# Kernel tuning notes

Hardware: AMD Instinct MI355X
Metric: run time of the kernel (lower is better)

The kernel has to match this reference:

```python
import jax, jax.numpy as jnp
import numpy as np

B, N, E = 2, 50000, 800000
IN_CH, SP_CH, OUT_CH, EDGE_CH = 64, 16, 32, 1


def _xavier(k, shape):
    scale = (2.0 / (shape[0] + shape[1])) ** 0.5
    return jax.random.normal(k, shape, dtype=jnp.float32) * scale


def setup_inputs() -> dict:
    key = jax.random.key(0)
    ks = jax.random.split(key, 20)
    return {
        "X": jax.random.normal(ks[0], (B, N, IN_CH), dtype=jnp.float32),
        "edge_index0": jax.random.randint(ks[1], (2, E), 0, N),
        "edge_index1": jax.random.randint(ks[2], (2, E), 0, N),
        "edge_weight0": jax.random.uniform(ks[3], (E, EDGE_CH), dtype=jnp.float32),
        "edge_weight1": jax.random.uniform(ks[4], (E, EDGE_CH), dtype=jnp.float32),
        "res_n_id0": jnp.arange(N),
        "res_n_id1": jnp.arange(N),
        # conv1 params (in=IN_CH, out=SP_CH)
        "value1": _xavier(ks[5], (IN_CH, SP_CH)),
        "key1": _xavier(ks[6], (SP_CH, SP_CH)),
        "query1": _xavier(ks[7], (SP_CH, SP_CH)),
        "we1": _xavier(ks[8], (EDGE_CH, SP_CH)),
        "att_w1": _xavier(ks[9], (3 * SP_CH, 1)),
        "att_b1": jnp.zeros((1,), jnp.float32),
        "cat_w1": _xavier(ks[10], (2 * SP_CH, SP_CH)),
        "cat_b1": jnp.zeros((SP_CH,), jnp.float32),
        # conv2 params (in=SP_CH, out=OUT_CH)
        "value2": _xavier(ks[11], (SP_CH, OUT_CH)),
        "key2": _xavier(ks[12], (OUT_CH, OUT_CH)),
        "query2": _xavier(ks[13], (OUT_CH, OUT_CH)),
        "we2": _xavier(ks[14], (EDGE_CH, OUT_CH)),
        "att_w2": _xavier(ks[15], (3 * OUT_CH, 1)),
        "att_b2": jnp.zeros((1,), jnp.float32),
        "cat_w2": _xavier(ks[16], (2 * OUT_CH, OUT_CH)),
        "cat_b2": jnp.zeros((OUT_CH,), jnp.float32),
    }


def _egnn_conv(Xs, Xd, ei, ef, value, key_w, query_w, we, att_w, att_b, cat_w, cat_b):
    # Xs: [B,Ns,Cin] source nodes, Xd: [B,Nd,Cin] dest nodes, ei: [2,E], ef: [E,edge_ch]
    xs = Xs @ value                       # [B,Ns,C]
    xd = Xd @ value                       # [B,Nd,C]
    e = ef @ we                           # [E,C]
    xj = xs[:, ei[0]]                     # [B,E,C] source gather
    xi = xd[:, ei[1]]                     # [B,E,C] dest gather
    q = xj @ query_w                      # note: original code names are swapped; kept faithful
    k = xi @ key_w
    att_in = jnp.concatenate([k, q, jnp.broadcast_to(e, q.shape)], axis=-1)  # [B,E,3C]
    att = jax.nn.sigmoid(att_in @ att_w + att_b)      # [B,E,1]
    msg = att * xj * jax.nn.sigmoid(e)                # [B,E,C]
    aggr = jnp.zeros(xd.shape, xd.dtype).at[:, ei[1]].add(msg)  # scatter-add over dest
    upd = jnp.concatenate([xd, aggr], axis=-1) @ cat_w + cat_b  # [B,Nd,C]
    return xd + jax.nn.relu(upd)


def reference(X, edge_index0, edge_index1, edge_weight0, edge_weight1,
              res_n_id0, res_n_id1,
              value1, key1, query1, we1, att_w1, att_b1, cat_w1, cat_b1,
              value2, key2, query2, we2, att_w2, att_b2, cat_w2, cat_b2):
    X1 = _egnn_conv(X, X[:, res_n_id0], edge_index0, edge_weight0,
                    value1, key1, query1, we1, att_w1, att_b1, cat_w1, cat_b1)
    X1 = jax.nn.leaky_relu(X1)  # negative_slope 0.01, matches torch default
    X2 = _egnn_conv(X1, X1[:, res_n_id1], edge_index1, edge_weight1,
                    value2, key2, query2, we2, att_w2, att_b2, cat_w2, cat_b2)
    return X2
```

## Files before the change

kernel.cpp:

```cpp
#include <hip/hip_runtime.h>
#include <hip/hip_fp16.h>

#define BB   2
#define NN   50000
#define EE   800000
#define INCH 64
#define C1   16
#define C2   32
#define NB   (BB*NN)

#define W1S   6
#define W2S   5
#define NBK1  ((NN + 63) >> 6)
#define NBK2  ((NN + 31) >> 5)
#define NBKT  (NBK1 + NBK2)
#define EB    4096
#define TPB   1024
#define NEBLK ((2*EE + EB - 1) / EB)

#define OFF_XS1   0
#define OFF_XS2   (OFF_XS1 + NB*C1/2)
#define OFF_DOTK1 (OFF_XS2 + NB*C2/2)
#define OFF_DOTQ1 (OFF_DOTK1 + NB)
#define OFF_DOTK2 (OFF_DOTQ1 + NB)
#define OFF_DOTQ2 (OFF_DOTK2 + NB)
#define OFF_AG1   (OFF_DOTQ2 + NB)
#define OFF_AG2   (OFF_AG1 + NN*32)
#define OFF_BTOT  (OFF_AG2 + NN*64)
#define OFF_BBASE (OFF_BTOT + NBKT)
#define OFF_START (OFF_BBASE + NBKT)
#define OFF_DEG   (OFF_START + 2*NN)
#define OFF_SC    (OFF_DEG + 2*NN)
#define OFF_RECS2 (OFF_SC + 2)
#define OFF_REGION (OFF_RECS2 + 2*EE*2)
#define OFF_RECS   OFF_REGION
#define OFF_BCNT   (OFF_REGION + 2*EE*2)
#define OFF_PREC   OFF_REGION

__device__ __forceinline__ float sigmoidf(float x) {
    return __builtin_amdgcn_rcpf(1.0f + __expf(-x));
}

__global__ void k_sc(const float* __restrict__ we1, const float* __restrict__ aw1,
                     const float* __restrict__ we2, const float* __restrict__ aw2,
                     float* __restrict__ sc) {
    if (threadIdx.x == 0) {
        float e = 0.f;
        for (int j = 0; j < C1; ++j) e += we1[j] * aw1[2*C1+j];
        sc[0] = e;
    }
    if (threadIdx.x == 1) {
        float e = 0.f;
        for (int j = 0; j < C2; ++j) e += we2[j] * aw2[2*C2+j];
        sc[1] = e;
    }
}

__global__ __launch_bounds__(TPB) void k_cnt(
        const int* __restrict__ ei0, const int* __restrict__ ei1,
        unsigned* __restrict__ blockCnt) {
    __shared__ unsigned h[NBKT];
    int tid = threadIdx.x;
    for (int i = tid; i < NBKT; i += TPB) h[i] = 0u;
    __syncthreads();
    int base = blockIdx.x * EB;
#pragma unroll
    for (int j = 0; j < EB/TPB; ++j) {
        int t = base + j*TPB + tid;
        if (t < 2*EE) {
            int bkt;
            if (t < EE) { int dst = ei0[EE + t];      bkt = dst >> W1S; }
            else        { int dst = ei1[EE + t - EE]; bkt = NBK1 + (dst >> W2S); }
            atomicAdd(&h[bkt], 1u);
        }
    }
    __syncthreads();
    unsigned* o = blockCnt + (size_t)blockIdx.x * NBKT;
    for (int i = tid; i < NBKT; i += TPB) o[i] = h[i];
}

__global__ __launch_bounds__(512) void k_scanBkt(
        unsigned* __restrict__ blockCnt, unsigned* __restrict__ bktTot) {
    __shared__ unsigned s[512];
    int tid = threadIdx.x;
    int bkt = blockIdx.x;
    unsigned v = (tid < NEBLK) ? blockCnt[(size_t)tid * NBKT + bkt] : 0u;
    s[tid] = v;
    __syncthreads();
    for (int o = 1; o < 512; o <<= 1) {
        unsigned t = (tid >= o) ? s[tid - o] : 0u;
        __syncthreads();
        s[tid] += t;
        __syncthreads();
    }
    if (tid < NEBLK) blockCnt[(size_t)tid * NBKT + bkt] = s[tid] - v;
    if (tid == 511) bktTot[bkt] = s[511];
}

__global__ __launch_bounds__(1024) void k_scanTot(
        const unsigned* __restrict__ bktTot, unsigned* __restrict__ bucketBase) {
    __shared__ unsigned s[1024];
    int tid = threadIdx.x;
    int base = tid * 3;
    unsigned a0 = (base + 0 < NBKT) ? bktTot[base + 0] : 0u;
    unsigned a1 = (base + 1 < NBKT) ? bktTot[base + 1] : 0u;
    unsigned a2 = (base + 2 < NBKT) ? bktTot[base + 2] : 0u;
    unsigned l = a0 + a1 + a2;
    s[tid] = l;
    __syncthreads();
    for (int o = 1; o < 1024; o <<= 1) {
        unsigned t = (tid >= o) ? s[tid - o] : 0u;
        __syncthreads();
        s[tid] += t;
        __syncthreads();
    }
    unsigned ex = s[tid] - l;
    if (base + 0 < NBKT) bucketBase[base + 0] = ex;
    if (base + 1 < NBKT) bucketBase[base + 1] = ex + a0;
    if (base + 2 < NBKT) bucketBase[base + 2] = ex + a0 + a1;
}

__global__ __launch_bounds__(TPB) void k_permute(
        const int* __restrict__ ei0, const int* __restrict__ ei1,
        const float* __restrict__ ew0, const float* __restrict__ ew1,
        const unsigned* __restrict__ blockOff, const unsigned* __restrict__ bucketBase,
        uint2* __restrict__ recs) {
    __shared__ unsigned off[NBKT];
    __shared__ unsigned cur[NBKT];
    int tid = threadIdx.x;
    const unsigned* bo = blockOff + (size_t)blockIdx.x * NBKT;
    for (int i = tid; i < NBKT; i += TPB) { off[i] = bo[i] + bucketBase[i]; cur[i] = 0u; }
    __syncthreads();
    int base = blockIdx.x * EB;
#pragma unroll
    for (int j = 0; j < EB/TPB; ++j) {
        int t = base + j*TPB + tid;
        if (t >= 2*EE) break;
        int bkt, dl, src; float ef;
        if (t < EE) {
            int dst = ei0[EE + t];
            bkt = dst >> W1S; dl = dst & 63;
            src = ei0[t]; ef = ew0[t];
        } else {
            int e = t - EE;
            int dst = ei1[EE + e];
            bkt = NBK1 + (dst >> W2S); dl = dst & 31;
            src = ei1[e]; ef = ew1[e];
        }
        unsigned pos = off[bkt] + atomicAdd(&cur[bkt], 1u);
        recs[pos] = make_uint2((unsigned)src | ((unsigned)dl << 16), __float_as_uint(ef));
    }
}

__global__ __launch_bounds__(256) void k_sortb(
        const uint2* __restrict__ recs, const unsigned* __restrict__ bktTot,
        const unsigned* __restrict__ bucketBase,
        uint2* __restrict__ recs2, unsigned* __restrict__ startA,
        unsigned* __restrict__ degA) {
    __shared__ unsigned h[64], sOff[64], cur[64];
    int tid = threadIdx.x;
    int bkt = blockIdx.x;
    int lay1 = (bkt < NBK1) ? 1 : 0;
    int ndl  = lay1 ? 64 : 32;
    int nodeBase = lay1 ? (bkt << W1S) : ((bkt - NBK1) << W2S);
    int layOff   = lay1 ? 0 : NN;
    if (tid < 64) h[tid] = 0u;
    __syncthreads();
    unsigned cnt = bktTot[bkt], base = bucketBase[bkt];
    for (unsigned i = tid; i < cnt; i += 256)
        atomicAdd(&h[recs[base + i].x >> 16], 1u);
    __syncthreads();
    if (tid == 0) {
        unsigned run = 0;
        for (int d = 0; d < ndl; ++d) { sOff[d] = run; run += h[d]; }
    }
    __syncthreads();
    if (tid < ndl) {
        cur[tid] = sOff[tid];
        int node = nodeBase + tid;
        if (node < NN) {
            startA[layOff + node] = base + sOff[tid];
            degA[layOff + node]   = h[tid];
        }
    }
    __syncthreads();
    for (unsigned i = tid; i < cnt; i += 256) {
        uint2 r = recs[base + i];
        unsigned dl  = r.x >> 16;
        unsigned src = r.x & 0xffffu;
        unsigned pos = atomicAdd(&cur[dl], 1u);
        unsigned dst = (unsigned)nodeBase + dl;
        recs2[base + pos] = make_uint2(src | (dst << 16), r.y);
    }
}

__global__ __launch_bounds__(256) void k_value1(
        const float* __restrict__ X, const float* __restrict__ value1,
        const float* __restrict__ key1, const float* __restrict__ query1,
        const float* __restrict__ aw1,
        __half* __restrict__ xs1h, float* __restrict__ dotk1, float* __restrict__ dotq1) {
    __shared__ float W[INCH*C1];
    __shared__ float KV[C1], QV[C1];
    int tid = threadIdx.x;
    for (int i = tid; i < INCH*C1; i += 256) W[i] = value1[i];
    if (tid < C1) {
        float kv = 0.f, qv = 0.f;
#pragma unroll
        for (int j = 0; j < C1; ++j) {
            kv += key1[tid*C1+j]   * aw1[j];
            qv += query1[tid*C1+j] * aw1[C1+j];
        }
        KV[tid] = kv; QV[tid] = qv;
    }
    __syncthreads();
    int bn = blockIdx.x * 256 + tid;
    if (bn >= NB) return;
    int b = (bn >= NN) ? 1 : 0;
    int node = bn - b*NN;
    const float4* Xr = (const float4*)(X + (size_t)bn * INCH);
    float acc[C1];
#pragma unroll
    for (int j = 0; j < C1; ++j) acc[j] = 0.f;
#pragma unroll
    for (int v = 0; v < 16; ++v) {
        float4 p = Xr[v];
        float x4[4] = {p.x, p.y, p.z, p.w};
#pragma unroll
        for (int h = 0; h < 4; ++h) {
            int i = v*4 + h;
            float xv = x4[h];
#pragma unroll
            for (int j = 0; j < C1; ++j) acc[j] += xv * W[i*C1+j];
        }
    }
    float dk = 0.f, dq = 0.f;
#pragma unroll
    for (int j = 0; j < C1; ++j) { dk += acc[j]*KV[j]; dq += acc[j]*QV[j]; }
    __half* o = xs1h + ((size_t)node * C1) * 2 + b;
#pragma unroll
    for (int j = 0; j < C1; ++j) o[2*j] = __float2half_rn(acc[j]);
    dotk1[node*2 + b] = dk; dotq1[node*2 + b] = dq;
}

__global__ __launch_bounds__(256) void k_prep(
        const uint2* __restrict__ recs2seg, const float* __restrict__ dotk,
        const float* __restrict__ dotq, const float* __restrict__ ab,
        const float* __restrict__ sc, int scIdx, uint2* __restrict__ prec) {
    int e = blockIdx.x * 256 + threadIdx.x;
    uint2 r = recs2seg[e];
    int src = r.x & 0xffff, dst = r.x >> 16;
    float ef = __uint_as_float(r.y);
    float eb = ef * sc[scIdx] + ab[0];
    float2 dk = *(const float2*)(dotk + dst*2);
    float2 dq = *(const float2*)(dotq + src*2);
    float p0 = sigmoidf(dk.x + dq.x + eb);
    float p1 = sigmoidf(dk.y + dq.y + eb);
    unsigned pu = __builtin_bit_cast(unsigned, __floats2half2_rn(p0, p1));
    unsigned eu = (unsigned)__half_as_ushort(__float2half_rn(ef));
    prec[e] = make_uint2((unsigned)src | (pu << 16),
                         (pu >> 16) | (eu << 16));
}

__global__ __launch_bounds__(256) void k_aggr1f(
        const uint2* __restrict__ prec, const float* __restrict__ we,
        const uint2* __restrict__ xsh,
        const unsigned* __restrict__ startA, const unsigned* __restrict__ degA,
        float* __restrict__ aggrf) {
    int t = blockIdx.x * 256 + threadIdx.x;
    int node = t >> 3, cp = t & 7;
    if (node >= NN) return;
    unsigned s = startA[node];
    unsigned n = degA[node];
    float w0 = we[2*cp], w1 = we[2*cp+1];
    float a0 = 0.f, a1 = 0.f, a2 = 0.f, a3 = 0.f;
    uint2 r_n = make_uint2(0u, 0u); uint2 xr_n = make_uint2(0u, 0u);
    if (n > 0) {
        r_n = prec[s];
        xr_n = xsh[(size_t)(r_n.x & 0xffff)*8 + cp];
    }
    for (unsigned i = 0; i < n; ++i) {
        uint2 r = r_n; uint2 xr = xr_n;
        if (i + 1 < n) {
            r_n = prec[s + i + 1];
            xr_n = xsh[(size_t)(r_n.x & 0xffff)*8 + cp];
        }
        float p0 = __half2float(__ushort_as_half((unsigned short)(r.x >> 16)));
        float p1 = __half2float(__ushort_as_half((unsigned short)(r.y & 0xffff)));
        float ef = __half2float(__ushort_as_half((unsigned short)(r.y >> 16)));
        float se0 = sigmoidf(ef * w0);
        float se1 = sigmoidf(ef * w1);
        float2 f0 = __half22float2(__builtin_bit_cast(__half2, xr.x));
        float2 f1 = __half22float2(__builtin_bit_cast(__half2, xr.y));
        a0 += p0 * se0 * f0.x;
        a1 += p1 * se0 * f0.y;
        a2 += p0 * se1 * f1.x;
        a3 += p1 * se1 * f1.y;
    }
    ((float4*)aggrf)[(size_t)node*8 + cp] = make_float4(a0, a1, a2, a3);
}

__global__ __launch_bounds__(256) void k_update1(
        const float* __restrict__ cat_w, const float* __restrict__ cat_b,
        const float* __restrict__ value2,
        const float* __restrict__ key2, const float* __restrict__ query2,
        const float* __restrict__ aw2,
        const __half* __restrict__ xs1h, const float* __restrict__ aggr1f,
        __half* __restrict__ xs2h, float* __restrict__ dotk2, float* __restrict__ dotq2) {
    __shared__ float CW[2*C1*C1];
    __shared__ float CB[C1];
    __shared__ float V2[C1*C2];
    __shared__ float KV[C2], QV[C2];
    int tid = threadIdx.x;
    for (int i = tid; i < 2*C1*C1; i += 256) CW[i] = cat_w[i];
    for (int i = tid; i < C1*C2;   i += 256) V2[i] = value2[i];
    if (tid < C1) CB[tid] = cat_b[tid];
    if (tid < C2) {
        float kv = 0.f;
#pragma unroll
        for (int j = 0; j < C2; ++j) kv += key2[tid*C2+j] * aw2[j];
        KV[tid] = kv;
    } else if (tid < 2*C2) {
        int c = tid - C2;
        float qv = 0.f;
#pragma unroll
        for (int j = 0; j < C2; ++j) qv += query2[c*C2+j] * aw2[C2+j];
        QV[c] = qv;
    }
    __syncthreads();
    int bn = blockIdx.x * 256 + tid;
    if (bn >= NB) return;
    int b = (bn >= NN) ? 1 : 0;
    int node = bn - b*NN;
    const __half* xr = xs1h + ((size_t)node*C1)*2 + b;
    const float* agp = aggr1f + (size_t)node*32;
    float xd[C1], ag[C1];
#pragma unroll
    for (int i = 0; i < C1; ++i) xd[i] = __half2float(xr[2*i]);
#pragma unroll
    for (int i = 0; i < C1; ++i) ag[i] = agp[(i>>1)*4 + (i&1)*2 + b];
    float x1[C1];
#pragma unroll
    for (int j = 0; j < C1; ++j) {
        float u = CB[j];
#pragma unroll
        for (int i = 0; i < C1; ++i) {
            u += xd[i] * CW[i*C1 + j];
            u += ag[i] * CW[(C1+i)*C1 + j];
        }
        float o = xd[j] + fmaxf(u, 0.f);
        x1[j] = (o > 0.f) ? o : 0.01f * o;
    }
    float o2[C2];
#pragma unroll
    for (int k = 0; k < C2; ++k) o2[k] = 0.f;
#pragma unroll
    for (int j = 0; j < C1; ++j) {
        float xv = x1[j];
#pragma unroll
        for (int k = 0; k < C2; ++k) o2[k] += xv * V2[j*C2 + k];
    }
    float dk = 0.f, dq = 0.f;
#pragma unroll
    for (int k = 0; k < C2; ++k) { dk += o2[k]*KV[k]; dq += o2[k]*QV[k]; }
    __half* o = xs2h + ((size_t)node*C2)*2 + b;
#pragma unroll
    for (int k = 0; k < C2; ++k) o[2*k] = __float2half_rn(o2[k]);
    dotk2[node*2 + b] = dk; dotq2[node*2 + b] = dq;
}

__global__ __launch_bounds__(256) void k_aggr2f(
        const uint2* __restrict__ prec, const float* __restrict__ we,
        const uint2* __restrict__ xsh,
        const unsigned* __restrict__ startA, const unsigned* __restrict__ degA,
        float* __restrict__ aggrf) {
    int t = blockIdx.x * 256 + threadIdx.x;
    int node = t >> 4, cp = t & 15;
    if (node >= NN) return;
    unsigned s = startA[NN + node] - EE;
    unsigned n = degA[NN + node];
    float w0 = we[2*cp], w1 = we[2*cp+1];
    float a0 = 0.f, a1 = 0.f, a2 = 0.f, a3 = 0.f;
    uint2 r_n = make_uint2(0u, 0u); uint2 xr_n = make_uint2(0u, 0u);
    if (n > 0) {
        r_n = prec[s];
        xr_n = xsh[(size_t)(r_n.x & 0xffff)*16 + cp];
    }
    for (unsigned i = 0; i < n; ++i) {
        uint2 r = r_n; uint2 xr = xr_n;
        if (i + 1 < n) {
            r_n = prec[s + i + 1];
            xr_n = xsh[(size_t)(r_n.x & 0xffff)*16 + cp];
        }
        float p0 = __half2float(__ushort_as_half((unsigned short)(r.x >> 16)));
        float p1 = __half2float(__ushort_as_half((unsigned short)(r.y & 0xffff)));
        float ef = __half2float(__ushort_as_half((unsigned short)(r.y >> 16)));
        float se0 = sigmoidf(ef * w0);
        float se1 = sigmoidf(ef * w1);
        float2 f0 = __half22float2(__builtin_bit_cast(__half2, xr.x));
        float2 f1 = __half22float2(__builtin_bit_cast(__half2, xr.y));
        a0 += p0 * se0 * f0.x;
        a1 += p1 * se0 * f0.y;
        a2 += p0 * se1 * f1.x;
        a3 += p1 * se1 * f1.y;
    }
    ((float4*)aggrf)[(size_t)node*16 + cp] = make_float4(a0, a1, a2, a3);
}

__global__ __launch_bounds__(256) void k_update2(
        const float* __restrict__ cat_w, const float* __restrict__ cat_b,
        const __half* __restrict__ xs2h, const float* __restrict__ aggr2f,
        float* __restrict__ out) {
    __shared__ float CW[2*C2*C2];
    __shared__ float CB[C2];
    int tid = threadIdx.x;
    for (int i = tid; i < 2*C2*C2; i += 256) CW[i] = cat_w[i];
    if (tid < C2) CB[tid] = cat_b[tid];
    __syncthreads();
    int bn = blockIdx.x * 256 + tid;
    if (bn >= NB) return;
    int b = (bn >= NN) ? 1 : 0;
    int node = bn - b*NN;
    const __half* xr = xs2h + ((size_t)node*C2)*2 + b;
    const float* agp = aggr2f + (size_t)node*64;
    float xd[C2], ag[C2];
#pragma unroll
    for (int i = 0; i < C2; ++i) xd[i] = __half2float(xr[2*i]);
#pragma unroll
    for (int i = 0; i < C2; ++i) ag[i] = agp[(i>>1)*4 + (i&1)*2 + b];
    float o[C2];
#pragma unroll
    for (int k = 0; k < C2; ++k) {
        float u = CB[k];
#pragma unroll
        for (int i = 0; i < C2; ++i) {
            u += xd[i] * CW[i*C2 + k];
            u += ag[i] * CW[(C2+i)*C2 + k];
        }
        o[k] = xd[k] + fmaxf(u, 0.f);
    }
    float4* dst = (float4*)(out + (size_t)bn * C2);
#pragma unroll
    for (int v = 0; v < 8; ++v)
        dst[v] = make_float4(o[4*v], o[4*v+1], o[4*v+2], o[4*v+3]);
}

extern "C" void kernel_launch(void* const* d_in, const int* in_sizes, int n_in,
                              void* d_out, int out_size, void* d_ws, size_t ws_size,
                              hipStream_t stream) {
    const float* X      = (const float*)d_in[0];
    const int*   ei0    = (const int*)d_in[1];
    const int*   ei1    = (const int*)d_in[2];
    const float* ew0    = (const float*)d_in[3];
    const float* ew1    = (const float*)d_in[4];
    const float* value1 = (const float*)d_in[7];
    const float* key1   = (const float*)d_in[8];
    const float* query1 = (const float*)d_in[9];
    const float* we1    = (const float*)d_in[10];
    const float* aw1    = (const float*)d_in[11];
    const float* ab1    = (const float*)d_in[12];
    const float* cw1    = (const float*)d_in[13];
    const float* cb1    = (const float*)d_in[14];
    const float* value2 = (const float*)d_in[15];
    const float* key2   = (const float*)d_in[16];
    const float* query2 = (const float*)d_in[17];
    const float* we2    = (const float*)d_in[18];
    const float* aw2    = (const float*)d_in[19];
    const float* ab2    = (const float*)d_in[20];
    const float* cw2    = (const float*)d_in[21];
    const float* cb2    = (const float*)d_in[22];
    float* ws  = (float*)d_ws;
    float* out = (float*)d_out;

    __half* xs1h = (__half*)(ws + OFF_XS1);
    __half* xs2h = (__half*)(ws + OFF_XS2);
    float* aggr1f = ws + OFF_AG1;
    float* aggr2f = ws + OFF_AG2;
    unsigned* blockCnt   = (unsigned*)(ws + OFF_BCNT);
    unsigned* bktTot     = (unsigned*)(ws + OFF_BTOT);
    unsigned* bucketBase = (unsigned*)(ws + OFF_BBASE);
    unsigned* startA     = (unsigned*)(ws + OFF_START);
    unsigned* degA       = (unsigned*)(ws + OFF_DEG);
    uint2*    recs2      = (uint2*)(ws + OFF_RECS2);
    uint2*    recs       = (uint2*)(ws + OFF_RECS);
    uint2*    prec       = (uint2*)(ws + OFF_PREC);

    k_sc<<<1, 64, 0, stream>>>(we1, aw1, we2, aw2, ws + OFF_SC);

    k_value1<<<(NB+255)/256, 256, 0, stream>>>(X, value1, key1, query1, aw1,
                                               xs1h, ws + OFF_DOTK1, ws + OFF_DOTQ1);

    k_cnt<<<NEBLK, TPB, 0, stream>>>(ei0, ei1, blockCnt);
    k_scanBkt<<<NBKT, 512, 0, stream>>>(blockCnt, bktTot);
    k_scanTot<<<1, 1024, 0, stream>>>(bktTot, bucketBase);
    k_permute<<<NEBLK, TPB, 0, stream>>>(ei0, ei1, ew0, ew1,
                                         blockCnt, bucketBase, recs);
    k_sortb<<<NBKT, 256, 0, stream>>>(recs, bktTot, bucketBase,
                                      recs2, startA, degA);

    k_prep<<<EE/256, 256, 0, stream>>>(recs2, ws + OFF_DOTK1, ws + OFF_DOTQ1,
                                       ab1, ws + OFF_SC, 0, prec);
    k_aggr1f<<<(NN*8+255)/256, 256, 0, stream>>>(prec, we1, (const uint2*)xs1h,
                                                 startA, degA, aggr1f);
    k_update1<<<(NB+255)/256, 256, 0, stream>>>(cw1, cb1, value2, key2, query2, aw2,
                                                xs1h, aggr1f,
                                                xs2h, ws + OFF_DOTK2, ws + OFF_DOTQ2);

    k_prep<<<EE/256, 256, 0, stream>>>(recs2 + EE, ws + OFF_DOTK2, ws + OFF_DOTQ2,
                                       ab2, ws + OFF_SC, 1, prec);
    k_aggr2f<<<(NN*16+255)/256, 256, 0, stream>>>(prec, we2, (const uint2*)xs2h,
                                                  startA, degA, aggr2f);
    k_update2<<<(NB+255)/256, 256, 0, stream>>>(cw2, cb2, xs2h, aggr2f, out);
}
```

Before: 327.4 us.

## Precompute per-edge sigmoid edge gates and split each node's edges across two lanes

Adds a k_prese kernel that computes the per-edge, per-channel sigmoid(ef*we) gates once and stores them as packed half2 in sorted edge order. The aggregation kernels read these gates instead of recomputing exp/rcp per edge. They also give each node twice as many threads, with each half taking alternate edges, and combine the halves with a shuffle. The gate array is large (EE*8 and EE*16 words), so the exp work it removes is traded for extra global writes and reads plus two extra launches.

```diff
diff --git a/kernel.cpp b/kernel.cpp
--- a/kernel.cpp
+++ b/kernel.cpp
@@ -36,6 +36,7 @@
 #define OFF_RECS   OFF_REGION
 #define OFF_BCNT   (OFF_REGION + 2*EE*2)
 #define OFF_PREC   OFF_REGION
+#define OFF_SEV    (OFF_BCNT + NEBLK*NBKT)
 
 __device__ __forceinline__ float sigmoidf(float x) {
     return __builtin_amdgcn_rcpf(1.0f + __expf(-x));
@@ -261,42 +262,57 @@
                          (pu >> 16) | (eu << 16));
 }
 
+template<int LCP>
+__global__ __launch_bounds__(256) void k_prese(
+        const uint2* __restrict__ recs2seg, const float* __restrict__ we,
+        unsigned* __restrict__ sev) {
+    int t = blockIdx.x * 256 + threadIdx.x;
+    int e = t >> LCP, cp = t & ((1 << LCP) - 1);
+    float ef = __uint_as_float(recs2seg[e].y);
+    float se0 = sigmoidf(ef * we[2*cp]);
+    float se1 = sigmoidf(ef * we[2*cp+1]);
+    sev[t] = __builtin_bit_cast(unsigned, __floats2half2_rn(se0, se1));
+}
+
 __global__ __launch_bounds__(256) void k_aggr1f(
-        const uint2* __restrict__ prec, const float* __restrict__ we,
+        const uint2* __restrict__ prec, const unsigned* __restrict__ sev,
         const uint2* __restrict__ xsh,
         const unsigned* __restrict__ startA, const unsigned* __restrict__ degA,
         float* __restrict__ aggrf) {
     int t = blockIdx.x * 256 + threadIdx.x;
-    int node = t >> 3, cp = t & 7;
-    if (node >= NN) return;
+    int node = t >> 4, sub = t & 15, cp = sub & 7, h = sub >> 3;
     unsigned s = startA[node];
     unsigned n = degA[node];
-    float w0 = we[2*cp], w1 = we[2*cp+1];
     float a0 = 0.f, a1 = 0.f, a2 = 0.f, a3 = 0.f;
+    unsigned i = (unsigned)h;
     uint2 r_n = make_uint2(0u, 0u); uint2 xr_n = make_uint2(0u, 0u);
-    if (n > 0) {
-        r_n = prec[s];
+    unsigned sv_n = 0u;
+    if (i < n) {
+        r_n  = prec[s + i];
+        sv_n = sev[(size_t)(s + i)*8 + cp];
         xr_n = xsh[(size_t)(r_n.x & 0xffff)*8 + cp];
     }
-    for (unsigned i = 0; i < n; ++i) {
-        uint2 r = r_n; uint2 xr = xr_n;
-        if (i + 1 < n) {
-            r_n = prec[s + i + 1];
+    for (; i < n; i += 2) {
+        uint2 r = r_n; unsigned sv = sv_n; uint2 xr = xr_n;
+        if (i + 2 < n) {
+            r_n  = prec[s + i + 2];
+            sv_n = sev[(size_t)(s + i + 2)*8 + cp];
             xr_n = xsh[(size_t)(r_n.x & 0xffff)*8 + cp];
         }
         float p0 = __half2float(__ushort_as_half((unsigned short)(r.x >> 16)));
         float p1 = __half2float(__ushort_as_half((unsigned short)(r.y & 0xffff)));
-        float ef = __half2float(__ushort_as_half((unsigned short)(r.y >> 16)));
-        float se0 = sigmoidf(ef * w0);
-        float se1 = sigmoidf(ef * w1);
+        float2 se = __half22float2(__builtin_bit_cast(__half2, sv));
         float2 f0 = __half22float2(__builtin_bit_cast(__half2, xr.x));
         float2 f1 = __half22float2(__builtin_bit_cast(__half2, xr.y));
-        a0 += p0 * se0 * f0.x;
-        a1 += p1 * se0 * f0.y;
-        a2 += p0 * se1 * f1.x;
-        a3 += p1 * se1 * f1.y;
-    }
-    ((float4*)aggrf)[(size_t)node*8 + cp] = make_float4(a0, a1, a2, a3);
+        a0 += p0 * se.x * f0.x;
+        a1 += p1 * se.x * f0.y;
+        a2 += p0 * se.y * f1.x;
+        a3 += p1 * se.y * f1.y;
+    }
+    a0 += __shfl_xor(a0, 8); a1 += __shfl_xor(a1, 8);
+    a2 += __shfl_xor(a2, 8); a3 += __shfl_xor(a3, 8);
+    if (h == 0)
+        ((float4*)aggrf)[(size_t)node*8 + cp] = make_float4(a0, a1, a2, a3);
 }
 
 __global__ __launch_bounds__(256) void k_update1(
@@ -369,41 +385,44 @@
 }
 
 __global__ __launch_bounds__(256) void k_aggr2f(
-        const uint2* __restrict__ prec, const float* __restrict__ we,
+        const uint2* __restrict__ prec, const unsigned* __restrict__ sev,
         const uint2* __restrict__ xsh,
         const unsigned* __restrict__ startA, const unsigned* __restrict__ degA,
         float* __restrict__ aggrf) {
     int t = blockIdx.x * 256 + threadIdx.x;
-    int node = t >> 4, cp = t & 15;
-    if (node >= NN) return;
+    int node = t >> 5, sub = t & 31, cp = sub & 15, h = sub >> 4;
     unsigned s = startA[NN + node] - EE;
     unsigned n = degA[NN + node];
-    float w0 = we[2*cp], w1 = we[2*cp+1];
     float a0 = 0.f, a1 = 0.f, a2 = 0.f, a3 = 0.f;
+    unsigned i = (unsigned)h;
     uint2 r_n = make_uint2(0u, 0u); uint2 xr_n = make_uint2(0u, 0u);
-    if (n > 0) {
-        r_n = prec[s];
+    unsigned sv_n = 0u;
+    if (i < n) {
+        r_n  = prec[s + i];
+        sv_n = sev[(size_t)(s + i)*16 + cp];
         xr_n = xsh[(size_t)(r_n.x & 0xffff)*16 + cp];
     }
-    for (unsigned i = 0; i < n; ++i) {
-        uint2 r = r_n; uint2 xr = xr_n;
-        if (i + 1 < n) {
-            r_n = prec[s + i + 1];
+    for (; i < n; i += 2) {
+        uint2 r = r_n; unsigned sv = sv_n; uint2 xr = xr_n;
+        if (i + 2 < n) {
+            r_n  = prec[s + i + 2];
+            sv_n = sev[(size_t)(s + i + 2)*16 + cp];
             xr_n = xsh[(size_t)(r_n.x & 0xffff)*16 + cp];
         }
         float p0 = __half2float(__ushort_as_half((unsigned short)(r.x >> 16)));
         float p1 = __half2float(__ushort_as_half((unsigned short)(r.y & 0xffff)));
-        float ef = __half2float(__ushort_as_half((unsigned short)(r.y >> 16)));
-        float se0 = sigmoidf(ef * w0);
-        float se1 = sigmoidf(ef * w1);
+        float2 se = __half22float2(__builtin_bit_cast(__half2, sv));
         float2 f0 = __half22float2(__builtin_bit_cast(__half2, xr.x));
         float2 f1 = __half22float2(__builtin_bit_cast(__half2, xr.y));
-        a0 += p0 * se0 * f0.x;
-        a1 += p1 * se0 * f0.y;
-        a2 += p0 * se1 * f1.x;
-        a3 += p1 * se1 * f1.y;
-    }
-    ((float4*)aggrf)[(size_t)node*16 + cp] = make_float4(a0, a1, a2, a3);
+        a0 += p0 * se.x * f0.x;
+        a1 += p1 * se.x * f0.y;
+        a2 += p0 * se.y * f1.x;
+        a3 += p1 * se.y * f1.y;
+    }
+    a0 += __shfl_xor(a0, 16); a1 += __shfl_xor(a1, 16);
+    a2 += __shfl_xor(a2, 16); a3 += __shfl_xor(a3, 16);
+    if (h == 0)
+        ((float4*)aggrf)[(size_t)node*16 + cp] = make_float4(a0, a1, a2, a3);
 }
 
 __global__ __launch_bounds__(256) void k_update2(
@@ -483,6 +502,7 @@
     uint2*    recs2      = (uint2*)(ws + OFF_RECS2);
     uint2*    recs       = (uint2*)(ws + OFF_RECS);
     uint2*    prec       = (uint2*)(ws + OFF_PREC);
+    unsigned* sev        = (unsigned*)(ws + OFF_SEV);
 
     k_sc<<<1, 64, 0, stream>>>(we1, aw1, we2, aw2, ws + OFF_SC);
 
@@ -499,15 +519,17 @@
 
     k_prep<<<EE/256, 256, 0, stream>>>(recs2, ws + OFF_DOTK1, ws + OFF_DOTQ1,
                                        ab1, ws + OFF_SC, 0, prec);
-    k_aggr1f<<<(NN*8+255)/256, 256, 0, stream>>>(prec, we1, (const uint2*)xs1h,
-                                                 startA, degA, aggr1f);
+    k_prese<3><<<(EE*8)/256, 256, 0, stream>>>(recs2, we1, sev);
+    k_aggr1f<<<(NN*16)/256, 256, 0, stream>>>(prec, sev, (const uint2*)xs1h,
+                                              startA, degA, aggr1f);
     k_update1<<<(NB+255)/256, 256, 0, stream>>>(cw1, cb1, value2, key2, query2, aw2,
                                                 xs1h, aggr1f,
                                                 xs2h, ws + OFF_DOTK2, ws + OFF_DOTQ2);
 
     k_prep<<<EE/256, 256, 0, stream>>>(recs2 + EE, ws + OFF_DOTK2, ws + OFF_DOTQ2,
                                        ab2, ws + OFF_SC, 1, prec);
-    k_aggr2f<<<(NN*16+255)/256, 256, 0, stream>>>(prec, we2, (const uint2*)xs2h,
-                                                  startA, degA, aggr2f);
+    k_prese<4><<<(EE*16)/256, 256, 0, stream>>>(recs2 + EE, we2, sev);
+    k_aggr2f<<<(NN*32)/256, 256, 0, stream>>>(prec, sev, (const uint2*)xs2h,
+                                              startA, degA, aggr2f);
     k_update2<<<(NB+255)/256, 256, 0, stream>>>(cw2, cb2, xs2h, aggr2f, out);
 }
```

Result: slower. 362.9 us (+10.9%).
